# Optimization experiments

Measured on AMD Instinct MI355X. Metric: run time of the kernel, lower is better.

The kernel has to match this reference:

```python
import jax, jax.numpy as jnp
import numpy as np

H = 12       # heads
D = 768      # hidden size
DH = D // H  # head dim = 64
SCALE = 1.0 / jnp.sqrt(jnp.float32(DH))
LN_EPS = 1e-3  # keras LayerNormalization default epsilon


def setup_inputs() -> dict:
    key = jax.random.key(0)
    ks = jax.random.split(key, 8)
    B, L = 16, 512
    s = 0.02  # truncated-normal-ish init scale
    return {
        "x": jax.random.normal(ks[0], (B, L, D), jnp.float32),
        "mask": jnp.ones((B, L), jnp.int32),
        "Wq": jax.random.normal(ks[1], (D, D), jnp.float32) * s,
        "bq": jnp.zeros((D,), jnp.float32),
        "Wk": jax.random.normal(ks[2], (D, D), jnp.float32) * s,
        "bk": jnp.zeros((D,), jnp.float32),
        "Wv": jax.random.normal(ks[3], (D, D), jnp.float32) * s,
        "bv": jnp.zeros((D,), jnp.float32),
        "Wo": jax.random.normal(ks[4], (D, D), jnp.float32) * s,
        "bo": jnp.zeros((D,), jnp.float32),
        "gamma": jnp.ones((D,), jnp.float32),
        "beta": jnp.zeros((D,), jnp.float32),
    }


def reference(x, mask, Wq, bq, Wk, bk, Wv, bv, Wo, bo, gamma, beta):
    B, L, _ = x.shape
    # QKV projections, split into heads: [B, L, H, DH]
    q = (x @ Wq + bq).reshape(B, L, H, DH)
    k = (x @ Wk + bk).reshape(B, L, H, DH)
    v = (x @ Wv + bv).reshape(B, L, H, DH)
    # scaled dot-product scores: [B, H, Lq, Lk]
    scores = jnp.einsum('bqhd,bkhd->bhqk', q, k) * SCALE
    # key-side padding mask (mask==0 -> -inf)
    neg = jnp.float32(-1e9)
    scores = jnp.where(mask[:, None, None, :] > 0, scores, neg)
    p = jax.nn.softmax(scores, axis=-1)
    # dropout rate fixed to 0.0 -> identity
    ctx = jnp.einsum('bhqk,bkhd->bqhd', p, v).reshape(B, L, D)
    attn_out = ctx @ Wo + bo
    # residual + LayerNorm (keras default eps=1e-3)
    y = x + attn_out
    mu = jnp.mean(y, axis=-1, keepdims=True)
    var = jnp.mean(jnp.square(y - mu), axis=-1, keepdims=True)
    return gamma * (y - mu) * jax.lax.rsqrt(var + LN_EPS) + beta
```

## Files before the change

### kernel.cpp

```cpp
#include <hip/hip_runtime.h>
#include <math.h>

#define NH 12
#define DMODEL 768
#define DHEAD 64
#define BATCH 16
#define SEQ 512
#define NTOK (BATCH*SEQ)
#define ATTN_SCALE 0.125f
#define LN_EPS 1e-3f
#define PADP 72
#define NKT 12

typedef __attribute__((ext_vector_type(8))) short  bf16x8;
typedef __attribute__((ext_vector_type(4))) float  f32x4;

__device__ __forceinline__ unsigned short f2bf(float f) {
    unsigned int u = __float_as_uint(f);
    unsigned int r = (u + 0x7fffu + ((u >> 16) & 1u)) >> 16;
    return (unsigned short)r;
}

__device__ __forceinline__ void async_copy16(const void* g, void* l) {
    __builtin_amdgcn_global_load_lds((const __attribute__((address_space(1))) void*)g,
                                     (__attribute__((address_space(3))) void*)l,
                                     16, 0, 0);
}

#define SBAR() do { \
    __builtin_amdgcn_sched_barrier(0); \
    __builtin_amdgcn_s_barrier(); \
    __builtin_amdgcn_sched_barrier(0); \
} while (0)

#define VMW0() do { \
    __builtin_amdgcn_sched_barrier(0); \
    asm volatile("s_waitcnt vmcnt(0)" ::: "memory"); \
    __builtin_amdgcn_sched_barrier(0); \
} while (0)

__global__ __launch_bounds__(256) void prep_kernel(
    const float* __restrict__ x,
    const float* __restrict__ Wq, const float* __restrict__ Wk,
    const float* __restrict__ Wv, const float* __restrict__ Wo,
    unsigned short* __restrict__ xb,
    unsigned short* __restrict__ tq, unsigned short* __restrict__ tk,
    unsigned short* __restrict__ tv, unsigned short* __restrict__ to_)
{
    __shared__ float tile[32][33];
    const int bid = blockIdx.x;
    const int tid = threadIdx.x;

    if (bid < 6144) {
        int i = (bid * 256 + tid) * 4;
        const float4 v = *(const float4*)(x + i);
        unsigned long long pack =
              (unsigned long long)f2bf(v.x)
            | ((unsigned long long)f2bf(v.y) << 16)
            | ((unsigned long long)f2bf(v.z) << 32)
            | ((unsigned long long)f2bf(v.w) << 48);
        *(unsigned long long*)(xb + i) = pack;
        return;
    }

    const int t   = bid - 6144;
    const int zz  = t / 576;
    const int rem = t % 576;
    const float* W = (zz == 0) ? Wq : (zz == 1) ? Wk : (zz == 2) ? Wv : Wo;
    unsigned short* T = (zz == 0) ? tq : (zz == 1) ? tk : (zz == 2) ? tv : to_;

    const int bx = (rem / 24) * 32;
    const int by = (rem % 24) * 32;
    const int tx = tid & 31, ty = tid >> 5;

    #pragma unroll
    for (int i = 0; i < 32; i += 8)
        tile[ty + i][tx] = W[(size_t)(bx + ty + i) * DMODEL + by + tx];
    __syncthreads();
    #pragma unroll
    for (int i = 0; i < 32; i += 8)
        T[(size_t)(by + ty + i) * DMODEL + bx + tx] = f2bf(tile[tx][ty + i]);
}

#define QSTAGE(kt, sb) do { \
    const int _k0 = (kt) * 64; \
    _Pragma("unroll") \
    for (int _i = 0; _i < 4; ++_i) \
        async_copy16(aSrc + (size_t)_i * (8 * DMODEL) + _k0, &As[sb][(w * 4 + _i) * 512]); \
    _Pragma("unroll") \
    for (int _i = 0; _i < 4; ++_i) \
        async_copy16(bSrc + (size_t)_i * (64 * DMODEL) + _k0, &Bs[sb][(w + 8 * _i) * 512]); \
    if (w < 4) \
        async_copy16(bSrc + (size_t)4 * (64 * DMODEL) + _k0, &Bs[sb][(w + 32) * 512]); \
} while (0)

#define QTILE(t, c, o, hasNext) do { \
    if (hasNext) QSTAGE((t) + 1, o); \
    bf16x8 aF[4][2]; \
    _Pragma("unroll") \
    for (int _m = 0; _m < 4; ++_m) { \
        const int _row = wm * 64 + _m * 16 + l16; \
        aF[_m][0] = *(const bf16x8*)&As[c][_row * 64 + p0]; \
        aF[_m][1] = *(const bf16x8*)&As[c][_row * 64 + (p0 ^ 32)]; \
    } \
    _Pragma("unroll") \
    for (int _nh = 0; _nh < 3; ++_nh) { \
        bf16x8 bF[3][2]; \
        _Pragma("unroll") \
        for (int _n = 0; _n < 3; ++_n) { \
            const int _row = wn * 144 + (_nh * 3 + _n) * 16 + l16; \
            bF[_n][0] = *(const bf16x8*)&Bs[c][_row * 64 + p0]; \
            bF[_n][1] = *(const bf16x8*)&Bs[c][_row * 64 + (p0 ^ 32)]; \
        } \
        __builtin_amdgcn_s_setprio(1); \
        _Pragma("unroll") \
        for (int _k = 0; _k < 2; ++_k) \
          _Pragma("unroll") \
          for (int _m = 0; _m < 4; ++_m) \
            _Pragma("unroll") \
            for (int _n = 0; _n < 3; ++_n) \
              acc[_m][_nh * 3 + _n] = __builtin_amdgcn_mfma_f32_16x16x32_bf16( \
                  aF[_m][_k], bF[_n][_k], acc[_m][_nh * 3 + _n], 0, 0, 0); \
        __builtin_amdgcn_s_setprio(0); \
    } \
    if (hasNext) VMW0(); \
    SBAR(); \
} while (0)

__global__ __launch_bounds__(512, 2) void gemm_db_qkv(
    const unsigned short* __restrict__ xb, const unsigned short* __restrict__ wt,
    const float* __restrict__ bq, const float* __restrict__ bk, const float* __restrict__ bv,
    unsigned short* __restrict__ o0, unsigned short* __restrict__ o1,
    unsigned short* __restrict__ o2)
{
    __shared__ __align__(16) unsigned short As[2][256 * 64];
    __shared__ __align__(16) unsigned short Bs[2][288 * 64];

    const int orig = blockIdx.x;
    const int wg   = (orig & 7) * 32 + (orig >> 3);
    const int m0   = (wg >> 3) * 256;
    const int n0   = (wg & 7) * 288;

    const int tid  = threadIdx.x;
    const int lane = tid & 63;
    const int w    = tid >> 6;
    const int wm   = w >> 1, wn = w & 1;
    const int quad = lane >> 4;
    const int l16  = lane & 15;
    const int rloc = lane >> 3;
    const int csw  = (lane & 7) ^ rloc;
    const int p0   = (quad ^ (l16 & 7)) * 8;

    const unsigned short* aSrc = xb + (size_t)(m0 + w * 32 + rloc) * DMODEL + csw * 8;
    const unsigned short* bSrc = wt + (size_t)(n0 + w * 8  + rloc) * DMODEL + csw * 8;

    f32x4 acc[4][9] = {};

    QSTAGE(0, 0);
    VMW0();
    SBAR();

    #pragma unroll 1
    for (int tt = 0; tt < NKT / 2; ++tt) {
        QTILE(2 * tt,     0, 1, 1);
        QTILE(2 * tt + 1, 1, 0, (tt < NKT / 2 - 1));
    }

    #pragma unroll
    for (int nf = 0; nf < 9; ++nf) {
        const int ncg = n0 + wn * 144 + nf * 16 + l16;
        const int zz  = (ncg >= 1536) ? 2 : (ncg >= 768) ? 1 : 0;
        const int ncl = ncg - zz * 768;
        const int h = ncl >> 6, dh = ncl & 63;
        const float bval = ((zz == 0) ? bq : (zz == 1) ? bk : bv)[ncl];
        if (zz == 2) {
            #pragma unroll
            for (int mi = 0; mi < 4; ++mi) {
                const int mbase = m0 + wm * 64 + mi * 16 + quad * 4;
                const int bi = mbase >> 9, l = mbase & 511;
                unsigned long long pack = 0;
                #pragma unroll
                for (int r = 0; r < 4; ++r)
                    pack |= (unsigned long long)f2bf(acc[mi][nf][r] + bval) << (16 * r);
                *(unsigned long long*)(o2 + ((size_t)((bi * NH + h) * DHEAD + dh)) * SEQ + l) = pack;
            }
        } else {
            const float sc = (zz == 0) ? ATTN_SCALE : 1.0f;
            unsigned short* out = (zz == 0) ? o0 : o1;
            #pragma unroll
            for (int mi = 0; mi < 4; ++mi) {
                const int mbase = m0 + wm * 64 + mi * 16 + quad * 4;
                #pragma unroll
                for (int r = 0; r < 4; ++r) {
                    const int t = mbase + r;
                    const int bi = t >> 9, l = t & 511;
                    out[(size_t)((bi * NH + h) * SEQ + l) * DHEAD + dh] =
                        f2bf((acc[mi][nf][r] + bval) * sc);
                }
            }
        }
    }
}

#define FSTAGE_B(kb, h, pb) do { \
    _Pragma("unroll") \
    for (int _i = 0; _i < 6; ++_i) \
        async_copy16(wto + (size_t)((h) * 384 + _i * 64 + w * 8 + rloc) * DMODEL + (kb) * 64 + csw * 8, \
                     &Bb[pb][(_i * 64 + w * 8) * 64]); \
} while (0)

#define FSTAGE_A(kb, ab) do { \
    if (w < 4) \
        async_copy16(ctxb + (size_t)(m0 + w * 8 + rloc) * DMODEL + (kb) * 64 + csw * 8, \
                     &Ab[ab][(w * 8) * 64]); \
} while (0)

#define FPHASE(h, pb, ab) do { \
    bf16x8 aF[2][2], bF[3][2]; \
    _Pragma("unroll") \
    for (int _m = 0; _m < 2; ++_m) { \
        const int _row = _m * 16 + l16; \
        aF[_m][0] = *(const bf16x8*)&Ab[ab][_row * 64 + p0]; \
        aF[_m][1] = *(const bf16x8*)&Ab[ab][_row * 64 + (p0 ^ 32)]; \
    } \
    _Pragma("unroll") \
    for (int _n = 0; _n < 3; ++_n) { \
        const int _row = w * 48 + _n * 16 + l16; \
        bF[_n][0] = *(const bf16x8*)&Bb[pb][_row * 64 + p0]; \
        bF[_n][1] = *(const bf16x8*)&Bb[pb][_row * 64 + (p0 ^ 32)]; \
    } \
    __builtin_amdgcn_s_setprio(1); \
    _Pragma("unroll") \
    for (int _k = 0; _k < 2; ++_k) \
      _Pragma("unroll") \
      for (int _m = 0; _m < 2; ++_m) \
        _Pragma("unroll") \
        for (int _n = 0; _n < 3; ++_n) \
          acc[_m][(h) * 3 + _n] = __builtin_amdgcn_mfma_f32_16x16x32_bf16( \
              aF[_m][_k], bF[_n][_k], acc[_m][(h) * 3 + _n], 0, 0, 0); \
    __builtin_amdgcn_s_setprio(0); \
} while (0)

__global__ __launch_bounds__(512, 2) void oproj_ln_fused(
    const unsigned short* __restrict__ ctxb, const unsigned short* __restrict__ wto,
    const float* __restrict__ bo, const float* __restrict__ x,
    const float* __restrict__ gamma, const float* __restrict__ beta,
    float* __restrict__ out)
{
    __shared__ __align__(16) unsigned short Bb[2][384 * 64];
    __shared__ __align__(16) unsigned short Ab[2][32 * 64];
    __shared__ float rs[32][8], rs2[32][8];

    const int m0   = blockIdx.x * 32;
    const int tid  = threadIdx.x;
    const int lane = tid & 63;
    const int w    = tid >> 6;
    const int quad = lane >> 4;
    const int l16  = lane & 15;
    const int rloc = lane >> 3;
    const int csw  = (lane & 7) ^ rloc;
    const int p0   = (quad ^ (l16 & 7)) * 8;

    f32x4 acc[2][6] = {};

    FSTAGE_B(0, 0, 0);
    FSTAGE_A(0, 0);
    VMW0();
    SBAR();

    #pragma unroll 1
    for (int kb = 0; kb < NKT; ++kb) {
        FSTAGE_B(kb, 1, 1);
        if (kb + 1 < NKT) FSTAGE_A(kb + 1, (kb + 1) & 1);
        FPHASE(0, 0, kb & 1);
        VMW0();
        SBAR();
        if (kb + 1 < NKT) {
            FSTAGE_B(kb + 1, 0, 0);
            FPHASE(1, 1, kb & 1);
            VMW0();
            SBAR();
        } else {
            FPHASE(1, 1, kb & 1);
        }
    }

    float yv[2][6][4];
    float sp[2][4] = {}, sp2[2][4] = {};
    #pragma unroll
    for (int mi = 0; mi < 2; ++mi)
        #pragma unroll
        for (int j = 0; j < 6; ++j) {
            const int col = (j >= 3 ? 384 : 0) + w * 48 + (j % 3) * 16 + l16;
            const float bv_ = bo[col];
            #pragma unroll
            for (int rr = 0; rr < 4; ++rr) {
                const int row = mi * 16 + quad * 4 + rr;
                const float v = acc[mi][j][rr] + bv_
                              + x[(size_t)(m0 + row) * DMODEL + col];
                yv[mi][j][rr] = v;
                sp[mi][rr]  += v;
                sp2[mi][rr] += v * v;
            }
        }

    #pragma unroll
    for (int off = 1; off < 16; off <<= 1)
        #pragma unroll
        for (int mi = 0; mi < 2; ++mi)
            #pragma unroll
            for (int rr = 0; rr < 4; ++rr) {
                sp[mi][rr]  += __shfl_xor(sp[mi][rr],  off);
                sp2[mi][rr] += __shfl_xor(sp2[mi][rr], off);
            }

    if (l16 == 0)
        #pragma unroll
        for (int mi = 0; mi < 2; ++mi)
            #pragma unroll
            for (int rr = 0; rr < 4; ++rr) {
                const int row = mi * 16 + quad * 4 + rr;
                rs[row][w]  = sp[mi][rr];
                rs2[row][w] = sp2[mi][rr];
            }
    __syncthreads();

    float mu_[2][4], inv_[2][4];
    #pragma unroll
    for (int mi = 0; mi < 2; ++mi)
        #pragma unroll
        for (int rr = 0; rr < 4; ++rr) {
            const int row = mi * 16 + quad * 4 + rr;
            float ts = 0.f, ts2 = 0.f;
            #pragma unroll
            for (int ww = 0; ww < 8; ++ww) { ts += rs[row][ww]; ts2 += rs2[row][ww]; }
            const float mu  = ts * (1.f / DMODEL);
            const float var = ts2 * (1.f / DMODEL) - mu * mu;
            mu_[mi][rr]  = mu;
            inv_[mi][rr] = rsqrtf(var + LN_EPS);
        }

    #pragma unroll
    for (int mi = 0; mi < 2; ++mi)
        #pragma unroll
        for (int j = 0; j < 6; ++j) {
            const int col = (j >= 3 ? 384 : 0) + w * 48 + (j % 3) * 16 + l16;
            const float gm = gamma[col], bt = beta[col];
            #pragma unroll
            for (int rr = 0; rr < 4; ++rr) {
                const int row = mi * 16 + quad * 4 + rr;
                out[(size_t)(m0 + row) * DMODEL + col] =
                    gm * (yv[mi][j][rr] - mu_[mi][rr]) * inv_[mi][rr] + bt;
            }
        }
}

__global__ __launch_bounds__(256, 3) void attn_mfma_kernel(
    const unsigned short* __restrict__ q, const unsigned short* __restrict__ k,
    const unsigned short* __restrict__ vt, const int* __restrict__ mask,
    unsigned short* __restrict__ ctxb)
{
    __shared__ __align__(16) unsigned short Ks[2][64 * 64];
    __shared__ __align__(16) unsigned short Vs[2][64 * 64];
    __shared__ __align__(16) unsigned short Ps[2][64 * PADP];
    __shared__ float maskV[SEQ];

    const int tid  = threadIdx.x;
    const int lane = tid & 63;
    const int w    = tid >> 6;
    const int quad = lane >> 4;
    const int l16  = lane & 15;

    const int id = blockIdx.x;
    const int qt = id / (BATCH * NH);
    const int g  = id % (BATCH * NH);
    const int b  = g / NH, h = g % NH;
    const int q0 = qt * 128;

    const unsigned short* qp  = q  + ((size_t)(b * NH + h) * SEQ + q0) * DHEAD;
    const unsigned short* kp  = k  + (size_t)(b * NH + h) * SEQ * DHEAD;
    const unsigned short* vtp = vt + (size_t)(b * NH + h) * DHEAD * SEQ;

    const int rloc = lane >> 3;
    const int csw  = (lane & 7) ^ rloc;
    const int p0   = (quad ^ (l16 & 7)) * 8;

    #pragma unroll
    for (int ii = 0; ii < 2; ++ii) {
        const int inst = 2 * w + ii;
        async_copy16(kp  + (size_t)(inst * 8 + rloc) * DHEAD + csw * 8, &Ks[0][inst * 512]);
        async_copy16(vtp + (size_t)(inst * 8 + rloc) * SEQ + csw * 8,   &Vs[0][inst * 512]);
    }
    #pragma unroll
    for (int j = 0; j < 2; ++j) {
        const int idx = tid + 256 * j;
        maskV[idx] = (mask[b * SEQ + idx] > 0) ? 0.f : -1e9f;
    }

    bf16x8 aQ[2][2];
    #pragma unroll
    for (int qtl = 0; qtl < 2; ++qtl)
        #pragma unroll
        for (int ks = 0; ks < 2; ++ks)
            aQ[qtl][ks] = *(const bf16x8*)(qp + (size_t)(qtl * 64 + w * 16 + l16) * DHEAD
                                              + ks * 32 + quad * 8);

    bf16x8 ones;
    #pragma unroll
    for (int j = 0; j < 8; ++j) ones[j] = (short)0x3F80;

    f32x4 o[2][4] = {};
    f32x4 lsum[2] = {};
    const f32x4 zf = {0.f, 0.f, 0.f, 0.f};

    __syncthreads();

    #pragma unroll
    for (int it = 0; it < 8; ++it) {
        const int cur = it & 1;
        if (it + 1 < 8) {
            const int kt1 = (it + 1) * 64;
            #pragma unroll
            for (int ii = 0; ii < 2; ++ii) {
                const int inst = 2 * w + ii;
                async_copy16(kp  + (size_t)(kt1 + inst * 8 + rloc) * DHEAD + csw * 8,
                             &Ks[1 - cur][inst * 512]);
                async_copy16(vtp + (size_t)(inst * 8 + rloc) * SEQ + kt1 + csw * 8,
                             &Vs[1 - cur][inst * 512]);
            }
        }
        const int kt = it * 64;

        f32x4 s[2][4];
        #pragma unroll
        for (int ni = 0; ni < 4; ++ni) {
            bf16x8 bK0 = *(const bf16x8*)&Ks[cur][(ni * 16 + l16) * 64 + p0];
            bf16x8 bK1 = *(const bf16x8*)&Ks[cur][(ni * 16 + l16) * 64 + (p0 ^ 32)];
            #pragma unroll
            for (int qtl = 0; qtl < 2; ++qtl) {
                f32x4 t0 = __builtin_amdgcn_mfma_f32_16x16x32_bf16(aQ[qtl][0], bK0, zf, 0, 0, 0);
                s[qtl][ni] = __builtin_amdgcn_mfma_f32_16x16x32_bf16(aQ[qtl][1], bK1, t0, 0, 0, 0);
            }
        }

        #pragma unroll
        for (int ni = 0; ni < 4; ++ni) {
            const float mk = maskV[kt + ni * 16 + l16];
            #pragma unroll
            for (int qtl = 0; qtl < 2; ++qtl)
                #pragma unroll
                for (int r = 0; r < 4; ++r)
                    Ps[qtl][(w * 16 + quad * 4 + r) * PADP + ni * 16 + l16]
                        = (unsigned short)(__float_as_uint(__expf(s[qtl][ni][r] + mk)) >> 16);
        }

        bf16x8 aP[2][2];
        #pragma unroll
        for (int qtl = 0; qtl < 2; ++qtl) {
            #pragma unroll
            for (int ks = 0; ks < 2; ++ks)
                aP[qtl][ks] = *(const bf16x8*)&Ps[qtl][(w * 16 + l16) * PADP + quad * 8 + ks * 32];
            lsum[qtl] = __builtin_amdgcn_mfma_f32_16x16x32_bf16(aP[qtl][0], ones, lsum[qtl], 0, 0, 0);
            lsum[qtl] = __builtin_amdgcn_mfma_f32_16x16x32_bf16(aP[qtl][1], ones, lsum[qtl], 0, 0, 0);
        }

        #pragma unroll
        for (int ni = 0; ni < 4; ++ni) {
            bf16x8 bV0 = *(const bf16x8*)&Vs[cur][(ni * 16 + l16) * 64 + p0];
            bf16x8 bV1 = *(const bf16x8*)&Vs[cur][(ni * 16 + l16) * 64 + (p0 ^ 32)];
            #pragma unroll
            for (int qtl = 0; qtl < 2; ++qtl) {
                o[qtl][ni] = __builtin_amdgcn_mfma_f32_16x16x32_bf16(aP[qtl][0], bV0, o[qtl][ni], 0, 0, 0);
                o[qtl][ni] = __builtin_amdgcn_mfma_f32_16x16x32_bf16(aP[qtl][1], bV1, o[qtl][ni], 0, 0, 0);
            }
        }

        __syncthreads();
    }

    #pragma unroll
    for (int qtl = 0; qtl < 2; ++qtl)
        #pragma unroll
        for (int r = 0; r < 4; ++r) {
            const float inv = 1.f / lsum[qtl][r];
            const int tok = q0 + qtl * 64 + w * 16 + quad * 4 + r;
            #pragma unroll
            for (int ni = 0; ni < 4; ++ni)
                ctxb[(size_t)(b * SEQ + tok) * DMODEL + h * DHEAD + ni * 16 + l16]
                    = f2bf(o[qtl][ni][r] * inv);
        }
}

extern "C" void kernel_launch(void* const* d_in, const int* in_sizes, int n_in,
                              void* d_out, int out_size, void* d_ws, size_t ws_size,
                              hipStream_t stream) {
    const float* x     = (const float*)d_in[0];
    const int*   mask  = (const int*)  d_in[1];
    const float* Wq    = (const float*)d_in[2];
    const float* bq    = (const float*)d_in[3];
    const float* Wk    = (const float*)d_in[4];
    const float* bk    = (const float*)d_in[5];
    const float* Wv    = (const float*)d_in[6];
    const float* bv    = (const float*)d_in[7];
    const float* Wo    = (const float*)d_in[8];
    const float* bo    = (const float*)d_in[9];
    const float* gamma = (const float*)d_in[10];
    const float* beta  = (const float*)d_in[11];
    float* out = (float*)d_out;

    const size_t perTok = (size_t)NTOK * DMODEL;
    const size_t perW   = (size_t)DMODEL * DMODEL;

    unsigned short* xb   = (unsigned short*)d_ws;
    unsigned short* wtq  = xb + perTok;
    unsigned short* wtk  = wtq + perW;
    unsigned short* wtv  = wtk + perW;
    unsigned short* wto  = wtv + perW;
    unsigned short* qb   = wto + perW;
    unsigned short* kb   = qb + perTok;
    unsigned short* vb   = kb + perTok;
    unsigned short* ctxb = vb + perTok;

    prep_kernel<<<6144 + 2304, 256, 0, stream>>>(
        x, Wq, Wk, Wv, Wo, xb, wtq, wtk, wtv, wto);

    gemm_db_qkv<<<256, 512, 0, stream>>>(xb, wtq, bq, bk, bv, qb, kb, vb);

    attn_mfma_kernel<<<dim3((SEQ / 128) * BATCH * NH), 256, 0, stream>>>(
        qb, kb, vb, mask, ctxb);

    oproj_ln_fused<<<256, 512, 0, stream>>>(
        ctxb, wto, bo, x, gamma, beta, out);
}
```

Baseline: 191.8 us.

## Fuse all four stages into one persistent kernel with grid barriers

Replaces the four separate launches (prep, QKV GEMM, attention, out-proj+LN) with a single persistent 256-block kernel. Stages are separated by a software grid barrier built on atomics, and one shared-memory buffer is reused across stages. The aim is to remove launch gaps and tail effects between kernels. In exchange, attention now runs 512-thread blocks with each wave doing one 64-query tile over 3 passes instead of 768 separate blocks, which changes occupancy. It also relies on all 256 blocks being co-resident for the spin barrier to avoid deadlock.

```diff
diff --git a/kernel.cpp b/kernel.cpp
--- a/kernel.cpp
+++ b/kernel.cpp
@@ -11,6 +11,7 @@
 #define LN_EPS 1e-3f
 #define PADP 72
 #define NKT 12
+#define PERW 589824
 
 typedef __attribute__((ext_vector_type(8))) short  bf16x8;
 typedef __attribute__((ext_vector_type(4))) float  f32x4;
@@ -39,47 +40,25 @@
     __builtin_amdgcn_sched_barrier(0); \
 } while (0)
 
-__global__ __launch_bounds__(256) void prep_kernel(
-    const float* __restrict__ x,
-    const float* __restrict__ Wq, const float* __restrict__ Wk,
-    const float* __restrict__ Wv, const float* __restrict__ Wo,
-    unsigned short* __restrict__ xb,
-    unsigned short* __restrict__ tq, unsigned short* __restrict__ tk,
-    unsigned short* __restrict__ tv, unsigned short* __restrict__ to_)
-{
-    __shared__ float tile[32][33];
-    const int bid = blockIdx.x;
-    const int tid = threadIdx.x;
-
-    if (bid < 6144) {
-        int i = (bid * 256 + tid) * 4;
-        const float4 v = *(const float4*)(x + i);
-        unsigned long long pack =
-              (unsigned long long)f2bf(v.x)
-            | ((unsigned long long)f2bf(v.y) << 16)
-            | ((unsigned long long)f2bf(v.z) << 32)
-            | ((unsigned long long)f2bf(v.w) << 48);
-        *(unsigned long long*)(xb + i) = pack;
-        return;
+__device__ __forceinline__ void grid_barrier(unsigned* bar) {
+    __syncthreads();
+    if (threadIdx.x == 0) {
+        __threadfence();
+        unsigned* cnt = bar;
+        unsigned* gen = bar + 1;
+        const unsigned g = atomicAdd(gen, 0u);
+        const unsigned v = atomicAdd(cnt, 1u);
+        if (v == 255u) {
+            atomicExch(cnt, 0u);
+            __threadfence();
+            atomicAdd(gen, 1u);
+        } else {
+            while (atomicAdd(gen, 0u) == g)
+                __builtin_amdgcn_s_sleep(8);
+        }
+        __threadfence();
     }
-
-    const int t   = bid - 6144;
-    const int zz  = t / 576;
-    const int rem = t % 576;
-    const float* W = (zz == 0) ? Wq : (zz == 1) ? Wk : (zz == 2) ? Wv : Wo;
-    unsigned short* T = (zz == 0) ? tq : (zz == 1) ? tk : (zz == 2) ? tv : to_;
-
-    const int bx = (rem / 24) * 32;
-    const int by = (rem % 24) * 32;
-    const int tx = tid & 31, ty = tid >> 5;
-
-    #pragma unroll
-    for (int i = 0; i < 32; i += 8)
-        tile[ty + i][tx] = W[(size_t)(bx + ty + i) * DMODEL + by + tx];
     __syncthreads();
-    #pragma unroll
-    for (int i = 0; i < 32; i += 8)
-        T[(size_t)(by + ty + i) * DMODEL + bx + tx] = f2bf(tile[tx][ty + i]);
 }
 
 #define QSTAGE(kt, sb) do { \
@@ -127,81 +106,6 @@
     SBAR(); \
 } while (0)
 
-__global__ __launch_bounds__(512, 2) void gemm_db_qkv(
-    const unsigned short* __restrict__ xb, const unsigned short* __restrict__ wt,
-    const float* __restrict__ bq, const float* __restrict__ bk, const float* __restrict__ bv,
-    unsigned short* __restrict__ o0, unsigned short* __restrict__ o1,
-    unsigned short* __restrict__ o2)
-{
-    __shared__ __align__(16) unsigned short As[2][256 * 64];
-    __shared__ __align__(16) unsigned short Bs[2][288 * 64];
-
-    const int orig = blockIdx.x;
-    const int wg   = (orig & 7) * 32 + (orig >> 3);
-    const int m0   = (wg >> 3) * 256;
-    const int n0   = (wg & 7) * 288;
-
-    const int tid  = threadIdx.x;
-    const int lane = tid & 63;
-    const int w    = tid >> 6;
-    const int wm   = w >> 1, wn = w & 1;
-    const int quad = lane >> 4;
-    const int l16  = lane & 15;
-    const int rloc = lane >> 3;
-    const int csw  = (lane & 7) ^ rloc;
-    const int p0   = (quad ^ (l16 & 7)) * 8;
-
-    const unsigned short* aSrc = xb + (size_t)(m0 + w * 32 + rloc) * DMODEL + csw * 8;
-    const unsigned short* bSrc = wt + (size_t)(n0 + w * 8  + rloc) * DMODEL + csw * 8;
-
-    f32x4 acc[4][9] = {};
-
-    QSTAGE(0, 0);
-    VMW0();
-    SBAR();
-
-    #pragma unroll 1
-    for (int tt = 0; tt < NKT / 2; ++tt) {
-        QTILE(2 * tt,     0, 1, 1);
-        QTILE(2 * tt + 1, 1, 0, (tt < NKT / 2 - 1));
-    }
-
-    #pragma unroll
-    for (int nf = 0; nf < 9; ++nf) {
-        const int ncg = n0 + wn * 144 + nf * 16 + l16;
-        const int zz  = (ncg >= 1536) ? 2 : (ncg >= 768) ? 1 : 0;
-        const int ncl = ncg - zz * 768;
-        const int h = ncl >> 6, dh = ncl & 63;
-        const float bval = ((zz == 0) ? bq : (zz == 1) ? bk : bv)[ncl];
-        if (zz == 2) {
-            #pragma unroll
-            for (int mi = 0; mi < 4; ++mi) {
-                const int mbase = m0 + wm * 64 + mi * 16 + quad * 4;
-                const int bi = mbase >> 9, l = mbase & 511;
-                unsigned long long pack = 0;
-                #pragma unroll
-                for (int r = 0; r < 4; ++r)
-                    pack |= (unsigned long long)f2bf(acc[mi][nf][r] + bval) << (16 * r);
-                *(unsigned long long*)(o2 + ((size_t)((bi * NH + h) * DHEAD + dh)) * SEQ + l) = pack;
-            }
-        } else {
-            const float sc = (zz == 0) ? ATTN_SCALE : 1.0f;
-            unsigned short* out = (zz == 0) ? o0 : o1;
-            #pragma unroll
-            for (int mi = 0; mi < 4; ++mi) {
-                const int mbase = m0 + wm * 64 + mi * 16 + quad * 4;
-                #pragma unroll
-                for (int r = 0; r < 4; ++r) {
-                    const int t = mbase + r;
-                    const int bi = t >> 9, l = t & 511;
-                    out[(size_t)((bi * NH + h) * SEQ + l) * DHEAD + dh] =
-                        f2bf((acc[mi][nf][r] + bval) * sc);
-                }
-            }
-        }
-    }
-}
-
 #define FSTAGE_B(kb, h, pb) do { \
     _Pragma("unroll") \
     for (int _i = 0; _i < 6; ++_i) \
@@ -241,17 +145,22 @@
     __builtin_amdgcn_s_setprio(0); \
 } while (0)
 
-__global__ __launch_bounds__(512, 2) void oproj_ln_fused(
-    const unsigned short* __restrict__ ctxb, const unsigned short* __restrict__ wto,
-    const float* __restrict__ bo, const float* __restrict__ x,
+__global__ __launch_bounds__(512, 2) void mega_kernel(
+    const float* __restrict__ x, const int* __restrict__ mask,
+    const float* __restrict__ Wq, const float* __restrict__ bq,
+    const float* __restrict__ Wk, const float* __restrict__ bk,
+    const float* __restrict__ Wv, const float* __restrict__ bv,
+    const float* __restrict__ Wo, const float* __restrict__ bo,
     const float* __restrict__ gamma, const float* __restrict__ beta,
-    float* __restrict__ out)
+    unsigned short* __restrict__ xb, unsigned short* __restrict__ wt,
+    unsigned short* __restrict__ wto,
+    unsigned short* __restrict__ qb, unsigned short* __restrict__ kb,
+    unsigned short* __restrict__ vb, unsigned short* __restrict__ ctxb,
+    float* __restrict__ out, unsigned* __restrict__ bar)
 {
-    __shared__ __align__(16) unsigned short Bb[2][384 * 64];
-    __shared__ __align__(16) unsigned short Ab[2][32 * 64];
-    __shared__ float rs[32][8], rs2[32][8];
-
-    const int m0   = blockIdx.x * 32;
+    __shared__ __align__(16) char smem[139264];
+
+    const int bid  = blockIdx.x;
     const int tid  = threadIdx.x;
     const int lane = tid & 63;
     const int w    = tid >> 6;
@@ -261,234 +170,305 @@
     const int csw  = (lane & 7) ^ rloc;
     const int p0   = (quad ^ (l16 & 7)) * 8;
 
-    f32x4 acc[2][6] = {};
-
-    FSTAGE_B(0, 0, 0);
-    FSTAGE_A(0, 0);
-    VMW0();
-    SBAR();
-
-    #pragma unroll 1
-    for (int kb = 0; kb < NKT; ++kb) {
-        FSTAGE_B(kb, 1, 1);
-        if (kb + 1 < NKT) FSTAGE_A(kb + 1, (kb + 1) & 1);
-        FPHASE(0, 0, kb & 1);
+    {
+        #pragma unroll
+        for (int pass = 0; pass < 12; ++pass) {
+            const int i = ((pass * 256 + bid) * 512 + tid) * 4;
+            const float4 v = *(const float4*)(x + i);
+            unsigned long long pack =
+                  (unsigned long long)f2bf(v.x)
+                | ((unsigned long long)f2bf(v.y) << 16)
+                | ((unsigned long long)f2bf(v.z) << 32)
+                | ((unsigned long long)f2bf(v.w) << 48);
+            *(unsigned long long*)(xb + i) = pack;
+        }
+        const int u = tid >> 8, utid = tid & 255;
+        const int tx = utid & 31, ty = utid >> 5;
+        auto tileT = (float (*)[33])(smem + u * 4352);
+        for (int pass = 0; pass < 5; ++pass) {
+            const int task = pass * 512 + bid * 2 + u;
+            if (task < 2304) {
+                const int zz = task / 576, rem = task % 576;
+                const float* W = (zz == 0) ? Wq : (zz == 1) ? Wk : (zz == 2) ? Wv : Wo;
+                const int bx = (rem / 24) * 32, by = (rem % 24) * 32;
+                #pragma unroll
+                for (int i = 0; i < 32; i += 8)
+                    tileT[ty + i][tx] = W[(size_t)(bx + ty + i) * DMODEL + by + tx];
+            }
+            __syncthreads();
+            if (task < 2304) {
+                const int zz = task / 576, rem = task % 576;
+                unsigned short* T = (zz == 3) ? wto : wt + (size_t)zz * PERW;
+                const int bx = (rem / 24) * 32, by = (rem % 24) * 32;
+                #pragma unroll
+                for (int i = 0; i < 32; i += 8)
+                    T[(size_t)(by + ty + i) * DMODEL + bx + tx] = f2bf(tileT[tx][ty + i]);
+            }
+            __syncthreads();
+        }
+    }
+    grid_barrier(bar);
+
+    {
+        auto As = (unsigned short (*)[256 * 64])(void*)smem;
+        auto Bs = (unsigned short (*)[288 * 64])(void*)(smem + 65536);
+
+        const int wg = (bid & 7) * 32 + (bid >> 3);
+        const int m0 = (wg >> 3) * 256;
+        const int n0 = (wg & 7) * 288;
+        const int wm = w >> 1, wn = w & 1;
+
+        const unsigned short* aSrc = xb + (size_t)(m0 + w * 32 + rloc) * DMODEL + csw * 8;
+        const unsigned short* bSrc = wt + (size_t)(n0 + w * 8  + rloc) * DMODEL + csw * 8;
+
+        f32x4 acc[4][9] = {};
+
+        QSTAGE(0, 0);
         VMW0();
         SBAR();
-        if (kb + 1 < NKT) {
-            FSTAGE_B(kb + 1, 0, 0);
-            FPHASE(1, 1, kb & 1);
+
+        #pragma unroll 1
+        for (int tt = 0; tt < NKT / 2; ++tt) {
+            QTILE(2 * tt,     0, 1, 1);
+            QTILE(2 * tt + 1, 1, 0, (tt < NKT / 2 - 1));
+        }
+
+        #pragma unroll
+        for (int nf = 0; nf < 9; ++nf) {
+            const int ncg = n0 + wn * 144 + nf * 16 + l16;
+            const int zz  = (ncg >= 1536) ? 2 : (ncg >= 768) ? 1 : 0;
+            const int ncl = ncg - zz * 768;
+            const int h = ncl >> 6, dh = ncl & 63;
+            const float bval = ((zz == 0) ? bq : (zz == 1) ? bk : bv)[ncl];
+            if (zz == 2) {
+                #pragma unroll
+                for (int mi = 0; mi < 4; ++mi) {
+                    const int mbase = m0 + wm * 64 + mi * 16 + quad * 4;
+                    const int bi = mbase >> 9, l = mbase & 511;
+                    unsigned long long pack = 0;
+                    #pragma unroll
+                    for (int r = 0; r < 4; ++r)
+                        pack |= (unsigned long long)f2bf(acc[mi][nf][r] + bval) << (16 * r);
+                    *(unsigned long long*)(vb + ((size_t)((bi * NH + h) * DHEAD + dh)) * SEQ + l) = pack;
+                }
+            } else {
+                const float sc = (zz == 0) ? ATTN_SCALE : 1.0f;
+                unsigned short* o01 = (zz == 0) ? qb : kb;
+                #pragma unroll
+                for (int mi = 0; mi < 4; ++mi) {
+                    const int mbase = m0 + wm * 64 + mi * 16 + quad * 4;
+                    #pragma unroll
+                    for (int r = 0; r < 4; ++r) {
+                        const int t = mbase + r;
+                        const int bi = t >> 9, l = t & 511;
+                        o01[(size_t)((bi * NH + h) * SEQ + l) * DHEAD + dh] =
+                            f2bf((acc[mi][nf][r] + bval) * sc);
+                    }
+                }
+            }
+        }
+    }
+    grid_barrier(bar);
+
+    {
+        auto Ks = (unsigned short (*)[64 * 64])(void*)smem;
+        auto Vs = (unsigned short (*)[64 * 64])(void*)(smem + 16384);
+        unsigned short* Ps = (unsigned short*)(smem + 32768);
+        float* maskV = (float*)(smem + 51200);
+
+        bf16x8 ones;
+        #pragma unroll
+        for (int j = 0; j < 8; ++j) ones[j] = (short)0x3F80;
+        const f32x4 zf = {0.f, 0.f, 0.f, 0.f};
+
+        for (int t = 0; t < 3; ++t) {
+            const int id = t * 256 + bid;
+            const int qt = id / (BATCH * NH);
+            const int g  = id % (BATCH * NH);
+            const int b  = g / NH, h = g % NH;
+            const int q0 = qt * 128;
+
+            const unsigned short* qp  = qb + ((size_t)(b * NH + h) * SEQ + q0) * DHEAD;
+            const unsigned short* kp  = kb + (size_t)(b * NH + h) * SEQ * DHEAD;
+            const unsigned short* vtp = vb + (size_t)(b * NH + h) * DHEAD * SEQ;
+
+            async_copy16(kp  + (size_t)(w * 8 + rloc) * DHEAD + csw * 8, &Ks[0][w * 512]);
+            async_copy16(vtp + (size_t)(w * 8 + rloc) * SEQ + csw * 8,   &Vs[0][w * 512]);
+            maskV[tid] = (mask[b * SEQ + tid] > 0) ? 0.f : -1e9f;
+
+            bf16x8 aQ[2];
+            #pragma unroll
+            for (int ks = 0; ks < 2; ++ks)
+                aQ[ks] = *(const bf16x8*)(qp + (size_t)(w * 16 + l16) * DHEAD + ks * 32 + quad * 8);
+
+            f32x4 o[4] = {};
+            f32x4 lsum = {0.f, 0.f, 0.f, 0.f};
+
+            __syncthreads();
+
+            #pragma unroll
+            for (int it = 0; it < 8; ++it) {
+                const int cur = it & 1;
+                if (it + 1 < 8) {
+                    const int kt1 = (it + 1) * 64;
+                    async_copy16(kp  + (size_t)(kt1 + w * 8 + rloc) * DHEAD + csw * 8,
+                                 &Ks[1 - cur][w * 512]);
+                    async_copy16(vtp + (size_t)(w * 8 + rloc) * SEQ + kt1 + csw * 8,
+                                 &Vs[1 - cur][w * 512]);
+                }
+                const int kt = it * 64;
+
+                f32x4 s[4];
+                #pragma unroll
+                for (int ni = 0; ni < 4; ++ni) {
+                    bf16x8 bK0 = *(const bf16x8*)&Ks[cur][(ni * 16 + l16) * 64 + p0];
+                    bf16x8 bK1 = *(const bf16x8*)&Ks[cur][(ni * 16 + l16) * 64 + (p0 ^ 32)];
+                    f32x4 t0 = __builtin_amdgcn_mfma_f32_16x16x32_bf16(aQ[0], bK0, zf, 0, 0, 0);
+                    s[ni] = __builtin_amdgcn_mfma_f32_16x16x32_bf16(aQ[1], bK1, t0, 0, 0, 0);
+                }
+
+                #pragma unroll
+                for (int ni = 0; ni < 4; ++ni) {
+                    const float mk = maskV[kt + ni * 16 + l16];
+                    #pragma unroll
+                    for (int r = 0; r < 4; ++r)
+                        Ps[(w * 16 + quad * 4 + r) * PADP + ni * 16 + l16]
+                            = (unsigned short)(__float_as_uint(__expf(s[ni][r] + mk)) >> 16);
+                }
+
+                bf16x8 aP[2];
+                #pragma unroll
+                for (int ks = 0; ks < 2; ++ks)
+                    aP[ks] = *(const bf16x8*)&Ps[(w * 16 + l16) * PADP + quad * 8 + ks * 32];
+
+                lsum = __builtin_amdgcn_mfma_f32_16x16x32_bf16(aP[0], ones, lsum, 0, 0, 0);
+                lsum = __builtin_amdgcn_mfma_f32_16x16x32_bf16(aP[1], ones, lsum, 0, 0, 0);
+
+                #pragma unroll
+                for (int ni = 0; ni < 4; ++ni) {
+                    bf16x8 bV0 = *(const bf16x8*)&Vs[cur][(ni * 16 + l16) * 64 + p0];
+                    bf16x8 bV1 = *(const bf16x8*)&Vs[cur][(ni * 16 + l16) * 64 + (p0 ^ 32)];
+                    o[ni] = __builtin_amdgcn_mfma_f32_16x16x32_bf16(aP[0], bV0, o[ni], 0, 0, 0);
+                    o[ni] = __builtin_amdgcn_mfma_f32_16x16x32_bf16(aP[1], bV1, o[ni], 0, 0, 0);
+                }
+
+                __syncthreads();
+            }
+
+            #pragma unroll
+            for (int r = 0; r < 4; ++r) {
+                const float inv = 1.f / lsum[r];
+                const int tok = q0 + w * 16 + quad * 4 + r;
+                #pragma unroll
+                for (int ni = 0; ni < 4; ++ni)
+                    ctxb[(size_t)(b * SEQ + tok) * DMODEL + h * DHEAD + ni * 16 + l16]
+                        = f2bf(o[ni][r] * inv);
+            }
+        }
+    }
+    grid_barrier(bar);
+
+    {
+        auto Bb = (unsigned short (*)[384 * 64])(void*)smem;
+        auto Ab = (unsigned short (*)[32 * 64])(void*)(smem + 98304);
+        auto rs  = (float (*)[8])(void*)(smem + 106496);
+        auto rs2 = (float (*)[8])(void*)(smem + 107520);
+
+        const int m0 = bid * 32;
+
+        f32x4 acc[2][6] = {};
+
+        FSTAGE_B(0, 0, 0);
+        FSTAGE_A(0, 0);
+        VMW0();
+        SBAR();
+
+        #pragma unroll 1
+        for (int kb2 = 0; kb2 < NKT; ++kb2) {
+            FSTAGE_B(kb2, 1, 1);
+            if (kb2 + 1 < NKT) FSTAGE_A(kb2 + 1, (kb2 + 1) & 1);
+            FPHASE(0, 0, kb2 & 1);
             VMW0();
             SBAR();
-        } else {
-            FPHASE(1, 1, kb & 1);
-        }
-    }
-
-    float yv[2][6][4];
-    float sp[2][4] = {}, sp2[2][4] = {};
-    #pragma unroll
-    for (int mi = 0; mi < 2; ++mi)
-        #pragma unroll
-        for (int j = 0; j < 6; ++j) {
-            const int col = (j >= 3 ? 384 : 0) + w * 48 + (j % 3) * 16 + l16;
-            const float bv_ = bo[col];
+            if (kb2 + 1 < NKT) {
+                FSTAGE_B(kb2 + 1, 0, 0);
+                FPHASE(1, 1, kb2 & 1);
+                VMW0();
+                SBAR();
+            } else {
+                FPHASE(1, 1, kb2 & 1);
+            }
+        }
+
+        float yv[2][6][4];
+        float sp[2][4] = {}, sp2[2][4] = {};
+        #pragma unroll
+        for (int mi = 0; mi < 2; ++mi)
+            #pragma unroll
+            for (int j = 0; j < 6; ++j) {
+                const int col = (j >= 3 ? 384 : 0) + w * 48 + (j % 3) * 16 + l16;
+                const float bv_ = bo[col];
+                #pragma unroll
+                for (int rr = 0; rr < 4; ++rr) {
+                    const int row = mi * 16 + quad * 4 + rr;
+                    const float v = acc[mi][j][rr] + bv_
+                                  + x[(size_t)(m0 + row) * DMODEL + col];
+                    yv[mi][j][rr] = v;
+                    sp[mi][rr]  += v;
+                    sp2[mi][rr] += v * v;
+                }
+            }
+
+        #pragma unroll
+        for (int off = 1; off < 16; off <<= 1)
+            #pragma unroll
+            for (int mi = 0; mi < 2; ++mi)
+                #pragma unroll
+                for (int rr = 0; rr < 4; ++rr) {
+                    sp[mi][rr]  += __shfl_xor(sp[mi][rr],  off);
+                    sp2[mi][rr] += __shfl_xor(sp2[mi][rr], off);
+                }
+
+        if (l16 == 0)
+            #pragma unroll
+            for (int mi = 0; mi < 2; ++mi)
+                #pragma unroll
+                for (int rr = 0; rr < 4; ++rr) {
+                    const int row = mi * 16 + quad * 4 + rr;
+                    rs[row][w]  = sp[mi][rr];
+                    rs2[row][w] = sp2[mi][rr];
+                }
+        __syncthreads();
+
+        float mu_[2][4], inv_[2][4];
+        #pragma unroll
+        for (int mi = 0; mi < 2; ++mi)
             #pragma unroll
             for (int rr = 0; rr < 4; ++rr) {
                 const int row = mi * 16 + quad * 4 + rr;
-                const float v = acc[mi][j][rr] + bv_
-                              + x[(size_t)(m0 + row) * DMODEL + col];
-                yv[mi][j][rr] = v;
-                sp[mi][rr]  += v;
-                sp2[mi][rr] += v * v;
-            }
-        }
-
-    #pragma unroll
-    for (int off = 1; off < 16; off <<= 1)
+                float ts = 0.f, ts2 = 0.f;
+                #pragma unroll
+                for (int ww = 0; ww < 8; ++ww) { ts += rs[row][ww]; ts2 += rs2[row][ww]; }
+                const float mu  = ts * (1.f / DMODEL);
+                const float var = ts2 * (1.f / DMODEL) - mu * mu;
+                mu_[mi][rr]  = mu;
+                inv_[mi][rr] = rsqrtf(var + LN_EPS);
+            }
+
         #pragma unroll
         for (int mi = 0; mi < 2; ++mi)
             #pragma unroll
-            for (int rr = 0; rr < 4; ++rr) {
-                sp[mi][rr]  += __shfl_xor(sp[mi][rr],  off);
-                sp2[mi][rr] += __shfl_xor(sp2[mi][rr], off);
-            }
-
-    if (l16 == 0)
-        #pragma unroll
-        for (int mi = 0; mi < 2; ++mi)
-            #pragma unroll
-            for (int rr = 0; rr < 4; ++rr) {
-                const int row = mi * 16 + quad * 4 + rr;
-                rs[row][w]  = sp[mi][rr];
-                rs2[row][w] = sp2[mi][rr];
-            }
-    __syncthreads();
-
-    float mu_[2][4], inv_[2][4];
-    #pragma unroll
-    for (int mi = 0; mi < 2; ++mi)
-        #pragma unroll
-        for (int rr = 0; rr < 4; ++rr) {
-            const int row = mi * 16 + quad * 4 + rr;
-            float ts = 0.f, ts2 = 0.f;
-            #pragma unroll
-            for (int ww = 0; ww < 8; ++ww) { ts += rs[row][ww]; ts2 += rs2[row][ww]; }
-            const float mu  = ts * (1.f / DMODEL);
-            const float var = ts2 * (1.f / DMODEL) - mu * mu;
-            mu_[mi][rr]  = mu;
-            inv_[mi][rr] = rsqrtf(var + LN_EPS);
-        }
-
-    #pragma unroll
-    for (int mi = 0; mi < 2; ++mi)
-        #pragma unroll
-        for (int j = 0; j < 6; ++j) {
-            const int col = (j >= 3 ? 384 : 0) + w * 48 + (j % 3) * 16 + l16;
-            const float gm = gamma[col], bt = beta[col];
-            #pragma unroll
-            for (int rr = 0; rr < 4; ++rr) {
-                const int row = mi * 16 + quad * 4 + rr;
-                out[(size_t)(m0 + row) * DMODEL + col] =
-                    gm * (yv[mi][j][rr] - mu_[mi][rr]) * inv_[mi][rr] + bt;
-            }
-        }
-}
-
-__global__ __launch_bounds__(256, 3) void attn_mfma_kernel(
-    const unsigned short* __restrict__ q, const unsigned short* __restrict__ k,
-    const unsigned short* __restrict__ vt, const int* __restrict__ mask,
-    unsigned short* __restrict__ ctxb)
-{
-    __shared__ __align__(16) unsigned short Ks[2][64 * 64];
-    __shared__ __align__(16) unsigned short Vs[2][64 * 64];
-    __shared__ __align__(16) unsigned short Ps[2][64 * PADP];
-    __shared__ float maskV[SEQ];
-
-    const int tid  = threadIdx.x;
-    const int lane = tid & 63;
-    const int w    = tid >> 6;
-    const int quad = lane >> 4;
-    const int l16  = lane & 15;
-
-    const int id = blockIdx.x;
-    const int qt = id / (BATCH * NH);
-    const int g  = id % (BATCH * NH);
-    const int b  = g / NH, h = g % NH;
-    const int q0 = qt * 128;
-
-    const unsigned short* qp  = q  + ((size_t)(b * NH + h) * SEQ + q0) * DHEAD;
-    const unsigned short* kp  = k  + (size_t)(b * NH + h) * SEQ * DHEAD;
-    const unsigned short* vtp = vt + (size_t)(b * NH + h) * DHEAD * SEQ;
-
-    const int rloc = lane >> 3;
-    const int csw  = (lane & 7) ^ rloc;
-    const int p0   = (quad ^ (l16 & 7)) * 8;
-
-    #pragma unroll
-    for (int ii = 0; ii < 2; ++ii) {
-        const int inst = 2 * w + ii;
-        async_copy16(kp  + (size_t)(inst * 8 + rloc) * DHEAD + csw * 8, &Ks[0][inst * 512]);
-        async_copy16(vtp + (size_t)(inst * 8 + rloc) * SEQ + csw * 8,   &Vs[0][inst * 512]);
+            for (int j = 0; j < 6; ++j) {
+                const int col = (j >= 3 ? 384 : 0) + w * 48 + (j % 3) * 16 + l16;
+                const float gm = gamma[col], bt = beta[col];
+                #pragma unroll
+                for (int rr = 0; rr < 4; ++rr) {
+                    const int row = mi * 16 + quad * 4 + rr;
+                    out[(size_t)(m0 + row) * DMODEL + col] =
+                        gm * (yv[mi][j][rr] - mu_[mi][rr]) * inv_[mi][rr] + bt;
+                }
+            }
     }
-    #pragma unroll
-    for (int j = 0; j < 2; ++j) {
-        const int idx = tid + 256 * j;
-        maskV[idx] = (mask[b * SEQ + idx] > 0) ? 0.f : -1e9f;
-    }
-
-    bf16x8 aQ[2][2];
-    #pragma unroll
-    for (int qtl = 0; qtl < 2; ++qtl)
-        #pragma unroll
-        for (int ks = 0; ks < 2; ++ks)
-            aQ[qtl][ks] = *(const bf16x8*)(qp + (size_t)(qtl * 64 + w * 16 + l16) * DHEAD
-                                              + ks * 32 + quad * 8);
-
-    bf16x8 ones;
-    #pragma unroll
-    for (int j = 0; j < 8; ++j) ones[j] = (short)0x3F80;
-
-    f32x4 o[2][4] = {};
-    f32x4 lsum[2] = {};
-    const f32x4 zf = {0.f, 0.f, 0.f, 0.f};
-
-    __syncthreads();
-
-    #pragma unroll
-    for (int it = 0; it < 8; ++it) {
-        const int cur = it & 1;
-        if (it + 1 < 8) {
-            const int kt1 = (it + 1) * 64;
-            #pragma unroll
-            for (int ii = 0; ii < 2; ++ii) {
-                const int inst = 2 * w + ii;
-                async_copy16(kp  + (size_t)(kt1 + inst * 8 + rloc) * DHEAD + csw * 8,
-                             &Ks[1 - cur][inst * 512]);
-                async_copy16(vtp + (size_t)(inst * 8 + rloc) * SEQ + kt1 + csw * 8,
-                             &Vs[1 - cur][inst * 512]);
-            }
-        }
-        const int kt = it * 64;
-
-        f32x4 s[2][4];
-        #pragma unroll
-        for (int ni = 0; ni < 4; ++ni) {
-            bf16x8 bK0 = *(const bf16x8*)&Ks[cur][(ni * 16 + l16) * 64 + p0];
-            bf16x8 bK1 = *(const bf16x8*)&Ks[cur][(ni * 16 + l16) * 64 + (p0 ^ 32)];
-            #pragma unroll
-            for (int qtl = 0; qtl < 2; ++qtl) {
-                f32x4 t0 = __builtin_amdgcn_mfma_f32_16x16x32_bf16(aQ[qtl][0], bK0, zf, 0, 0, 0);
-                s[qtl][ni] = __builtin_amdgcn_mfma_f32_16x16x32_bf16(aQ[qtl][1], bK1, t0, 0, 0, 0);
-            }
-        }
-
-        #pragma unroll
-        for (int ni = 0; ni < 4; ++ni) {
-            const float mk = maskV[kt + ni * 16 + l16];
-            #pragma unroll
-            for (int qtl = 0; qtl < 2; ++qtl)
-                #pragma unroll
-                for (int r = 0; r < 4; ++r)
-                    Ps[qtl][(w * 16 + quad * 4 + r) * PADP + ni * 16 + l16]
-                        = (unsigned short)(__float_as_uint(__expf(s[qtl][ni][r] + mk)) >> 16);
-        }
-
-        bf16x8 aP[2][2];
-        #pragma unroll
-        for (int qtl = 0; qtl < 2; ++qtl) {
-            #pragma unroll
-            for (int ks = 0; ks < 2; ++ks)
-                aP[qtl][ks] = *(const bf16x8*)&Ps[qtl][(w * 16 + l16) * PADP + quad * 8 + ks * 32];
-            lsum[qtl] = __builtin_amdgcn_mfma_f32_16x16x32_bf16(aP[qtl][0], ones, lsum[qtl], 0, 0, 0);
-            lsum[qtl] = __builtin_amdgcn_mfma_f32_16x16x32_bf16(aP[qtl][1], ones, lsum[qtl], 0, 0, 0);
-        }
-
-        #pragma unroll
-        for (int ni = 0; ni < 4; ++ni) {
-            bf16x8 bV0 = *(const bf16x8*)&Vs[cur][(ni * 16 + l16) * 64 + p0];
-            bf16x8 bV1 = *(const bf16x8*)&Vs[cur][(ni * 16 + l16) * 64 + (p0 ^ 32)];
-            #pragma unroll
-            for (int qtl = 0; qtl < 2; ++qtl) {
-                o[qtl][ni] = __builtin_amdgcn_mfma_f32_16x16x32_bf16(aP[qtl][0], bV0, o[qtl][ni], 0, 0, 0);
-                o[qtl][ni] = __builtin_amdgcn_mfma_f32_16x16x32_bf16(aP[qtl][1], bV1, o[qtl][ni], 0, 0, 0);
-            }
-        }
-
-        __syncthreads();
-    }
-
-    #pragma unroll
-    for (int qtl = 0; qtl < 2; ++qtl)
-        #pragma unroll
-        for (int r = 0; r < 4; ++r) {
-            const float inv = 1.f / lsum[qtl][r];
-            const int tok = q0 + qtl * 64 + w * 16 + quad * 4 + r;
-            #pragma unroll
-            for (int ni = 0; ni < 4; ++ni)
-                ctxb[(size_t)(b * SEQ + tok) * DMODEL + h * DHEAD + ni * 16 + l16]
-                    = f2bf(o[qtl][ni][r] * inv);
-        }
 }
 
 extern "C" void kernel_launch(void* const* d_in, const int* in_sizes, int n_in,
@@ -509,26 +489,19 @@
     float* out = (float*)d_out;
 
     const size_t perTok = (size_t)NTOK * DMODEL;
-    const size_t perW   = (size_t)DMODEL * DMODEL;
 
     unsigned short* xb   = (unsigned short*)d_ws;
     unsigned short* wtq  = xb + perTok;
-    unsigned short* wtk  = wtq + perW;
-    unsigned short* wtv  = wtk + perW;
-    unsigned short* wto  = wtv + perW;
-    unsigned short* qb   = wto + perW;
+    unsigned short* wto  = wtq + 3 * (size_t)PERW;
+    unsigned short* qb   = wto + PERW;
     unsigned short* kb   = qb + perTok;
     unsigned short* vb   = kb + perTok;
     unsigned short* ctxb = vb + perTok;
-
-    prep_kernel<<<6144 + 2304, 256, 0, stream>>>(
-        x, Wq, Wk, Wv, Wo, xb, wtq, wtk, wtv, wto);
-
-    gemm_db_qkv<<<256, 512, 0, stream>>>(xb, wtq, bq, bk, bv, qb, kb, vb);
-
-    attn_mfma_kernel<<<dim3((SEQ / 128) * BATCH * NH), 256, 0, stream>>>(
-        qb, kb, vb, mask, ctxb);
-
-    oproj_ln_fused<<<256, 512, 0, stream>>>(
-        ctxb, wto, bo, x, gamma, beta, out);
+    unsigned* bar = (unsigned*)(ctxb + perTok);
+
+    hipMemsetAsync(bar, 0, 8, stream);
+
+    mega_kernel<<<256, 512, 0, stream>>>(
+        x, mask, Wq, bq, Wk, bk, Wv, bv, Wo, bo, gamma, beta,
+        xb, wtq, wto, qb, kb, vb, ctxb, out, bar);
 }
```

Result: slower. 300.1 us (+56.4%).
